# Kernel optimization log

Hardware: AMD Instinct MI355X
Metric: run time of the kernel (lower is better)

## Reference

```python
import jax, jax.numpy as jnp
import numpy as np

NC = 80
NA = 3
NO = NC + 5  # 85
ANCHORS = jnp.array([[[10.,13.],[16.,30.],[33.,23.]],
                     [[30.,61.],[62.,45.],[59.,119.]],
                     [[116.,90.],[156.,198.],[373.,326.]]], dtype=jnp.float32)
STRIDES = (8.0, 16.0, 32.0)
CONF_THRES = 0.25
IOU_THRES = 0.45
NMS_TOPK = 1000   # fixed candidate count for jit-friendly NMS (YOLO caps at max_nms)
MAX_DET = 300
MAX_WH = 4096.0   # class-offset trick from non_max_suppression


def _decode(x, w, b, anchors, stride):
    # x: [B,C,ny,nx]; w: [255,C]; 1x1 conv == channel matmul
    B, _, ny, nx = x.shape
    y = jnp.einsum('bchw,oc->bohw', x, w) + b[None, :, None, None]
    y = y.reshape(B, NA, NO, ny, nx).transpose(0, 1, 3, 4, 2)  # [B,na,ny,nx,no]
    s = jax.nn.sigmoid(y)
    yv, xv = jnp.meshgrid(jnp.arange(ny, dtype=y.dtype), jnp.arange(nx, dtype=y.dtype), indexing='ij')
    grid = jnp.stack((xv, yv), -1) - 0.5                      # [ny,nx,2]
    xy = (s[..., :2] * 2.0 + grid[None, None]) * stride
    wh = (s[..., 2:4] * 2.0) ** 2 * (anchors * stride)[None, :, None, None, :]
    out = jnp.concatenate((xy, wh, s[..., 4:]), axis=-1)
    return out.reshape(B, NA * ny * nx, NO)


def _xywh2xyxy(x):
    xy, wh = x[..., :2], x[..., 2:4]
    return jnp.concatenate([xy - wh * 0.5, xy + wh * 0.5], axis=-1)


def _box_iou(a, b):
    lt = jnp.maximum(a[:, None, :2], b[None, :, :2])
    rb = jnp.minimum(a[:, None, 2:], b[None, :, 2:])
    wh = jnp.clip(rb - lt, 0.0)
    inter = wh[..., 0] * wh[..., 1]
    area_a = (a[:, 2] - a[:, 0]) * (a[:, 3] - a[:, 1])
    area_b = (b[:, 2] - b[:, 0]) * (b[:, 3] - b[:, 1])
    return inter / (area_a[:, None] + area_b[None, :] - inter + 1e-7)


def _nms_single(pred):
    # pred: [N, 85] -> dets [MAX_DET, 6] = (x1,y1,x2,y2,conf,cls), zero-padded
    boxes = _xywh2xyxy(pred[:, :4])
    obj = pred[:, 4]
    cls_conf = pred[:, 5:] * obj[:, None]          # class scores
    score = jnp.max(cls_conf, axis=-1)
    cls = jnp.argmax(cls_conf, axis=-1)
    score = jnp.where(score > CONF_THRES, score, 0.0)
    top_s, idx = jax.lax.top_k(score, NMS_TOPK)    # fixed candidate set
    b = boxes[idx]                                  # [K,4]
    c = cls[idx].astype(b.dtype)
    bo = b + (c * MAX_WH)[:, None]                  # class-aware offset
    iou = _box_iou(bo, bo)                          # [K,K]
    keep0 = top_s > CONF_THRES
    rng = jnp.arange(NMS_TOPK)

    def body(i, keep):
        sup = (iou[i] > IOU_THRES) & (rng > i)
        return jnp.where(keep[i], keep & (~sup), keep)

    keep = jax.lax.fori_loop(0, NMS_TOPK, body, keep0)
    final_s = jnp.where(keep, top_s, 0.0)
    fs, fi = jax.lax.top_k(final_s, MAX_DET)
    det = jnp.concatenate([b[fi], fs[:, None], c[fi][:, None]], axis=-1)  # [MAX_DET,6]
    det = jnp.where((fs > CONF_THRES)[:, None], det, 0.0)
    return det


def setup_inputs() -> dict:
    key = jax.random.key(0)
    ks = jax.random.split(key, 9)
    B = 16
    return {
        'x0': jax.random.normal(ks[0], (B, 128, 80, 80), jnp.float32),
        'x1': jax.random.normal(ks[1], (B, 256, 40, 40), jnp.float32),
        'x2': jax.random.normal(ks[2], (B, 512, 20, 20), jnp.float32),
        'w0': jax.random.normal(ks[3], (255, 128), jnp.float32) * 0.02,
        'b0': jax.random.normal(ks[4], (255,), jnp.float32) * 0.02,
        'w1': jax.random.normal(ks[5], (255, 256), jnp.float32) * 0.02,
        'b1': jax.random.normal(ks[6], (255,), jnp.float32) * 0.02,
        'w2': jax.random.normal(ks[7], (255, 512), jnp.float32) * 0.02,
        'b2': jax.random.normal(ks[8], (255,), jnp.float32) * 0.02,
    }


def reference(x0, x1, x2, w0, b0, w1, b1, w2, b2):
    z0 = _decode(x0, w0, b0, ANCHORS[0], STRIDES[0])
    z1 = _decode(x1, w1, b1, ANCHORS[1], STRIDES[1])
    z2 = _decode(x2, w2, b2, ANCHORS[2], STRIDES[2])
    pred = jnp.concatenate([z0, z1, z2], axis=1)   # [B, 25200, 85]
    dets = jax.vmap(_nms_single)(pred)             # [B, 300, 6]
    return dets, pred
```

## Files before the change

kernel.cpp:

```cpp
#include <hip/hip_runtime.h>
#include <cstdint>

#define BATCH   16
#define NCLS    80
#define NOUT    85
#define NANC    3
#define NCAND   25200
#define CONF    0.25f
#define IOUT    0.45f
#define TOPK    1000
#define MAXDET  300
#define MAXWH   4096.0f
#define CAPK    2048
#define NBH     520
#define XPAD    40

typedef __attribute__((ext_vector_type(8))) short short8;
typedef __attribute__((ext_vector_type(4))) float f32x4;
typedef unsigned int u32;

constexpr size_t SCORE_OFF = 0;
constexpr size_t CLS_OFF   = SCORE_OFF + (size_t)BATCH * NCAND * 4;
constexpr size_t THR_OFF   = CLS_OFF   + (size_t)BATCH * NCAND * 4;
constexpr size_t CNT_OFF   = THR_OFF   + 256;
constexpr size_t KEYS_OFF  = CNT_OFF   + 256;
constexpr size_t RS_OFF    = KEYS_OFF  + (size_t)BATCH * CAPK * 8;
constexpr size_t RBOX_OFF  = RS_OFF    + (size_t)BATCH * TOPK * 4;
constexpr size_t RBO_OFF   = RBOX_OFF  + (size_t)BATCH * TOPK * 16;
constexpr size_t RCLS_OFF  = RBO_OFF   + (size_t)BATCH * TOPK * 16;
constexpr size_t SUP_OFF   = RCLS_OFF  + (size_t)BATCH * TOPK * 4;
constexpr int NL0 = 255 * 128, NL1 = 255 * 256, NL2 = 255 * 512;
constexpr int WB0 = 0, WB1 = 3 * NL0, WB2 = 3 * NL0 + 3 * NL1;

__device__ __forceinline__ ushort bf16rn(float f) {
    uint32_t u = __float_as_uint(f);
    uint32_t r = u + 0x7FFFu + ((u >> 16) & 1u);
    return (ushort)(r >> 16);
}

__device__ __forceinline__ void split3(float v, ushort& s1, ushort& s2, ushort& s3) {
    ushort h1 = bf16rn(v);
    float f1 = __uint_as_float((uint32_t)h1 << 16);
    float r1 = v - f1;
    ushort h2 = bf16rn(r1);
    float f2 = __uint_as_float((uint32_t)h2 << 16);
    ushort h3 = bf16rn(r1 - f2);
    s1 = h1; s2 = h2; s3 = h3;
}

__device__ __forceinline__ void gl_lds16(const float* g, void* l) {
    __builtin_amdgcn_global_load_lds(
        (const __attribute__((address_space(1))) u32*)g,
        (__attribute__((address_space(3))) u32*)l, 16, 0, 0);
}

__global__ __launch_bounds__(256)
void wsplit_kernel(const float* __restrict__ w0, const float* __restrict__ w1,
                   const float* __restrict__ w2, ushort* __restrict__ wsp) {
    int i = blockIdx.x * 256 + threadIdx.x;
    if (i >= NL0 + NL1 + NL2) return;
    const float* src; int idx, base, NL;
    if (i < NL0)            { src = w0; idx = i;             base = WB0; NL = NL0; }
    else if (i < NL0 + NL1) { src = w1; idx = i - NL0;       base = WB1; NL = NL1; }
    else                    { src = w2; idx = i - NL0 - NL1; base = WB2; NL = NL2; }
    ushort s1, s2, s3;
    split3(src[idx], s1, s2, s3);
    wsp[base + idx]          = s1;
    wsp[base + NL + idx]     = s2;
    wsp[base + 2 * NL + idx] = s3;
}

template<int C, int NN>
__device__ __forceinline__ void decode_level(
    const float* __restrict__ xb,
    const ushort* __restrict__ w1p, const ushort* __restrict__ w2p,
    const ushort* __restrict__ w3p, const float* __restrict__ bias,
    float* __restrict__ predB, float* __restrict__ scoreB, int* __restrict__ clsB,
    int tile, int lvlOff, float stride,
    float aw0, float ah0, float aw1, float ah1, float aw2, float ah2,
    char* xsb0, char* xsb1, ushort* x1, ushort* x2, ushort* x3, float* staged)
{
    constexpr int NPOS = NN * NN;
    constexpr int NCHUNK = C / 32;
    constexpr int MAXOFF = C * NPOS - 4;
    const int tid  = threadIdx.x;
    const int lane = tid & 63;
    const int wid  = tid >> 6;
    const int l16  = lane >> 4;
    const int lr   = lane & 15;
    const int pos0 = tile * 32;

    f32x4 acc[4][2];
#pragma unroll
    for (int nf = 0; nf < 4; nf++)
#pragma unroll
        for (int pf = 0; pf < 2; pf++) acc[nf][pf] = (f32x4){0.f, 0.f, 0.f, 0.f};

    char* xsb[2] = {xsb0, xsb1};

    {
        int kc = tid >> 3;
        int p4 = (tid & 7) * 4;
        int off = kc * NPOS + pos0 + p4;
        off = off < MAXOFF ? off : MAXOFF;
        gl_lds16(xb + off, xsb[0] + tid * 16);
    }

    for (int c = 0; c < NCHUNK; c++) {
        float* xs = (float*)xsb[c & 1];
        __syncthreads();
        if (c + 1 < NCHUNK) {
            const int k0n = (c + 1) * 32;
            int kc = tid >> 3;
            int p4 = (tid & 7) * 4;
            int off = (k0n + kc) * NPOS + pos0 + p4;
            off = off < MAXOFF ? off : MAXOFF;
            gl_lds16(xb + off, xsb[(c + 1) & 1] + tid * 16);
        }
        if (tid < 128) {
            const int sp = tid & 31;
            const int wv = tid >> 5;
            short8 s1v, s2v, s3v;
#pragma unroll
            for (int j = 0; j < 8; j++) {
                float f = xs[(wv * 8 + j) * 32 + sp];
                ushort u1, u2, u3;
                split3(f, u1, u2, u3);
                s1v[j] = (short)u1; s2v[j] = (short)u2; s3v[j] = (short)u3;
            }
            int dst = sp * XPAD + ((wv ^ ((sp >> 2) & 3)) << 3);
            *(short8*)(x1 + dst) = s1v;
            *(short8*)(x2 + dst) = s2v;
            *(short8*)(x3 + dst) = s3v;
        }
        asm volatile("s_waitcnt lgkmcnt(0)" ::: "memory");
        __builtin_amdgcn_s_barrier();
        __builtin_amdgcn_sched_barrier(0);
        short8 b1[2], b2[2], b3[2];
#pragma unroll
        for (int pf = 0; pf < 2; pf++) {
            int pr = pf * 16 + lr;
            int off = pr * XPAD + ((l16 ^ ((pr >> 2) & 3)) << 3);
            b1[pf] = *(const short8*)(x1 + off);
            b2[pf] = *(const short8*)(x2 + off);
            b3[pf] = *(const short8*)(x3 + off);
        }
        const int k0 = c * 32;
#pragma unroll
        for (int nf = 0; nf < 4; nf++) {
            int o = wid * 64 + nf * 16 + lr;
            int oc = o < 255 ? o : 254;
            size_t aoff = (size_t)oc * C + k0 + l16 * 8;
            short8 A1 = *(const short8*)(w1p + aoff);
            short8 A2 = *(const short8*)(w2p + aoff);
            short8 A3 = *(const short8*)(w3p + aoff);
#pragma unroll
            for (int pf = 0; pf < 2; pf++) {
                acc[nf][pf] = __builtin_amdgcn_mfma_f32_16x16x32_bf16(A1, b1[pf], acc[nf][pf], 0, 0, 0);
                acc[nf][pf] = __builtin_amdgcn_mfma_f32_16x16x32_bf16(A1, b2[pf], acc[nf][pf], 0, 0, 0);
                acc[nf][pf] = __builtin_amdgcn_mfma_f32_16x16x32_bf16(A2, b1[pf], acc[nf][pf], 0, 0, 0);
                acc[nf][pf] = __builtin_amdgcn_mfma_f32_16x16x32_bf16(A2, b2[pf], acc[nf][pf], 0, 0, 0);
                acc[nf][pf] = __builtin_amdgcn_mfma_f32_16x16x32_bf16(A1, b3[pf], acc[nf][pf], 0, 0, 0);
                acc[nf][pf] = __builtin_amdgcn_mfma_f32_16x16x32_bf16(A3, b1[pf], acc[nf][pf], 0, 0, 0);
            }
        }
    }

    float bv[16];
#pragma unroll
    for (int nf = 0; nf < 4; nf++)
#pragma unroll
        for (int r = 0; r < 4; r++) {
            int o = wid * 64 + nf * 16 + l16 * 4 + r;
            bv[nf * 4 + r] = (o < 255) ? bias[o] : 0.f;
        }

    const float aw[3] = {aw0, aw1, aw2};
    const float ah[3] = {ah0, ah1, ah2};
    const int validP = (NPOS - pos0) < 32 ? (NPOS - pos0) : 32;

#pragma unroll
    for (int a = 0; a < 3; a++) {
        __syncthreads();
#pragma unroll
        for (int nf = 0; nf < 4; nf++) {
#pragma unroll
            for (int r = 0; r < 4; r++) {
                int o = wid * 64 + nf * 16 + l16 * 4 + r;
                int j = o - a * 85;
                if (o < 255 && j >= 0 && j < 85) {
#pragma unroll
                    for (int pf = 0; pf < 2; pf++) {
                        int p = pf * 16 + lr;
                        int pos = pos0 + p;
                        float y = acc[nf][pf][r] + bv[nf * 4 + r];
                        float s = 1.f / (1.f + __expf(-y));
                        float val;
                        if (j == 0) {
                            int gyi = pos / NN;
                            float gx = (float)(pos - gyi * NN);
                            val = (2.f * s + gx - 0.5f) * stride;
                        } else if (j == 1) {
                            float gy = (float)(pos / NN);
                            val = (2.f * s + gy - 0.5f) * stride;
                        } else if (j == 2) {
                            float t2 = 2.f * s; val = t2 * t2 * aw[a];
                        } else if (j == 3) {
                            float t2 = 2.f * s; val = t2 * t2 * ah[a];
                        } else {
                            val = s;
                        }
                        staged[p * 85 + j] = val;
                    }
                }
            }
        }
        __syncthreads();
        size_t base = ((size_t)lvlOff + (size_t)a * NPOS + pos0) * 85;
        if (validP == 32) {
            const float4* s4 = (const float4*)staged;
            float4* d4 = (float4*)(predB + base);
            for (int q = tid; q < (32 * 85 / 4); q += 256) d4[q] = s4[q];
        } else {
            int tot = validP * 85;
            for (int q = tid; q < tot; q += 256) predB[base + q] = staged[q];
        }
        int p = tid >> 3, c8 = tid & 7;
        if (p < validP) {
            int j0 = 5 + c8 * 10;
            float best = staged[p * 85 + j0];
            int bi = c8 * 10;
#pragma unroll
            for (int jj = 1; jj < 10; jj++) {
                float vv = staged[p * 85 + j0 + jj];
                if (vv > best) { best = vv; bi = c8 * 10 + jj; }
            }
#pragma unroll
            for (int d = 1; d < 8; d <<= 1) {
                float ov = __shfl_xor(best, d);
                int   oi = __shfl_xor(bi, d);
                if (ov > best || (ov == best && oi < bi)) { best = ov; bi = oi; }
            }
            if (c8 == 0) {
                float obj = staged[p * 85 + 4];
                float sc = obj * best;
                int cand = lvlOff + a * NPOS + pos0 + p;
                scoreB[cand] = (sc > CONF) ? sc : 0.f;
                clsB[cand] = bi;
            }
        }
    }
}

__global__ __launch_bounds__(256)
void decode_all_kernel(const float* __restrict__ x0, const float* __restrict__ x1,
                       const float* __restrict__ x2,
                       const float* __restrict__ b0, const float* __restrict__ b1,
                       const float* __restrict__ b2,
                       const ushort* __restrict__ wsp,
                       float* __restrict__ pred,
                       float* __restrict__ scoreArr, int* __restrict__ clsArr)
{
    __shared__ __align__(16) char smem[15872];
    char*   xsb0 = smem;
    char*   xsb1 = smem + 4096;
    ushort* p1   = (ushort*)(smem + 8192);
    ushort* p2   = (ushort*)(smem + 10752);
    ushort* p3   = (ushort*)(smem + 13312);
    float*  staged = (float*)smem;

    const int b = blockIdx.y;
    const int t = blockIdx.x;

    float* predB  = pred + (size_t)b * NCAND * 85;
    float* scoreB = scoreArr + (size_t)b * NCAND;
    int*   clsB   = clsArr + (size_t)b * NCAND;

    if (t < 13) {
        decode_level<512, 20>(x2 + (size_t)b * 512 * 400,
                              wsp + WB2, wsp + WB2 + NL2, wsp + WB2 + 2 * NL2, b2,
                              predB, scoreB, clsB, t, 24000, 32.f,
                              3712.f, 2880.f, 4992.f, 6336.f, 11936.f, 10432.f,
                              xsb0, xsb1, p1, p2, p3, staged);
    } else if (t < 63) {
        decode_level<256, 40>(x1 + (size_t)b * 256 * 1600,
                              wsp + WB1, wsp + WB1 + NL1, wsp + WB1 + 2 * NL1, b1,
                              predB, scoreB, clsB, t - 13, 19200, 16.f,
                              480.f, 976.f, 992.f, 720.f, 944.f, 1904.f,
                              xsb0, xsb1, p1, p2, p3, staged);
    } else {
        decode_level<128, 80>(x0 + (size_t)b * 128 * 6400,
                              wsp + WB0, wsp + WB0 + NL0, wsp + WB0 + 2 * NL0, b0,
                              predB, scoreB, clsB, t - 63, 0, 8.f,
                              80.f, 104.f, 128.f, 240.f, 264.f, 184.f,
                              xsb0, xsb1, p1, p2, p3, staged);
    }
}

__global__ __launch_bounds__(1024)
void select1_kernel(const float* __restrict__ score, const float* __restrict__ pred,
                    const int* __restrict__ clsArr, int* __restrict__ nArr,
                    float* __restrict__ rs, float* __restrict__ rbox,
                    float* __restrict__ rbo, float* __restrict__ rcls) {
    int img = blockIdx.x, tid = threadIdx.x;
    __shared__ uint64_t sk[CAPK];
    __shared__ uint32_t h[NBH];
    __shared__ uint32_t sfx[1024 + 1];
    __shared__ int bucketSh;
    __shared__ uint32_t cntS;
    for (int i = tid; i < NBH; i += 1024) h[i] = 0;
    for (int i = tid; i < CAPK; i += 1024) sk[i] = 0ull;
    if (tid == 0) cntS = 0u;
    __syncthreads();
    const float* s = score + (size_t)img * NCAND;
    for (int i = tid; i < NCAND; i += 1024) {
        float v = s[i];
        if (v > CONF) {
            int bk = (int)((__float_as_uint(v) >> 15) - 0x7D00u);
            bk = bk < 0 ? 0 : (bk >= NBH ? NBH - 1 : bk);
            atomicAdd(&h[bk], 1u);
        }
    }
    __syncthreads();
    sfx[tid] = (tid < NBH) ? h[tid] : 0u;
    if (tid == 0) sfx[1024] = 0u;
    __syncthreads();
    for (int off = 1; off < 1024; off <<= 1) {
        uint32_t v = sfx[tid] + ((tid + off < 1024) ? sfx[tid + off] : 0u);
        __syncthreads();
        sfx[tid] = v;
        __syncthreads();
    }
    uint32_t M = sfx[0];
    uint32_t target = M < TOPK ? M : TOPK;
    if (M > 0 && tid < NBH && sfx[tid] >= target && sfx[tid + 1] < target)
        bucketSh = tid;
    __syncthreads();
    uint32_t thr = (M == 0) ? 0xFFFFFFFFu : ((uint32_t)(bucketSh + 0x7D00) << 15);
    for (int i = tid; i < NCAND; i += 1024) {
        float v = s[i];
        if (v > CONF) {
            uint32_t bits = __float_as_uint(v);
            if (bits >= thr) {
                uint32_t pos = atomicAdd(&cntS, 1u);
                if (pos < CAPK)
                    sk[pos] = ((uint64_t)bits << 32) | (uint32_t)(~(uint32_t)i);
            }
        }
    }
    __syncthreads();
    uint32_t n = cntS < CAPK ? cntS : CAPK;
    for (int k = 2; k <= CAPK; k <<= 1)
        for (int j = k >> 1; j > 0; j >>= 1) {
            for (int i = tid; i < CAPK; i += 1024) {
                int l = i ^ j;
                if (l > i) {
                    uint64_t a = sk[i], b = sk[l];
                    bool descRegion = ((i & k) == 0);
                    bool sw = descRegion ? (a < b) : (a > b);
                    if (sw) { sk[i] = b; sk[l] = a; }
                }
            }
            __syncthreads();
        }
    for (int r = tid; r < TOPK; r += 1024) {
        float sc = 0.f; uint32_t idx = 0;
        if (r < (int)n) {
            uint64_t key = sk[r];
            sc = __uint_as_float((uint32_t)(key >> 32));
            idx = ~(uint32_t)key;
        }
        const float* pr = pred + ((size_t)img * NCAND + idx) * 85;
        float cx = pr[0], cy = pr[1], ww = pr[2], hh = pr[3];
        float x1 = cx - ww * 0.5f, y1 = cy - hh * 0.5f;
        float x2 = cx + ww * 0.5f, y2 = cy + hh * 0.5f;
        float c = (float)clsArr[(size_t)img * NCAND + idx];
        float off = c * MAXWH;
        size_t rb = ((size_t)img * TOPK + r) * 4;
        rbox[rb + 0] = x1; rbox[rb + 1] = y1; rbox[rb + 2] = x2; rbox[rb + 3] = y2;
        rbo[rb + 0] = x1 + off; rbo[rb + 1] = y1 + off;
        rbo[rb + 2] = x2 + off; rbo[rb + 3] = y2 + off;
        rs[(size_t)img * TOPK + r] = sc;
        rcls[(size_t)img * TOPK + r] = c;
    }
    if (tid == 0) nArr[img] = (int)(n < TOPK ? n : TOPK);
}

__global__ __launch_bounds__(256)
void sup_kernel(const float* __restrict__ rbo, uint64_t* __restrict__ sup) {
    int img = blockIdx.y;
    int wid = threadIdx.x >> 6, lane = threadIdx.x & 63;
    int i = blockIdx.x * 4 + wid;
    if (i >= TOPK) return;
    const float* bi_ = rbo + ((size_t)img * TOPK + i) * 4;
    float ax1 = bi_[0], ay1 = bi_[1], ax2 = bi_[2], ay2 = bi_[3];
    float areaA = (ax2 - ax1) * (ay2 - ay1);
    for (int w = 0; w < 16; w++) {
        int j = w * 64 + lane;
        bool cond = false;
        if (j < TOPK && j > i) {
            const float* bj = rbo + ((size_t)img * TOPK + j) * 4;
            float bx1 = bj[0], by1 = bj[1], bx2 = bj[2], by2 = bj[3];
            float ltx = fmaxf(ax1, bx1), lty = fmaxf(ay1, by1);
            float rbx = fminf(ax2, bx2), rby = fminf(ay2, by2);
            float iw = fmaxf(rbx - ltx, 0.f), ih = fmaxf(rby - lty, 0.f);
            float inter = iw * ih;
            float areaB = (bx2 - bx1) * (by2 - by1);
            float iou = inter / (areaA + areaB - inter + 1e-7f);
            cond = iou > IOUT;
        }
        unsigned long long m = __ballot(cond);
        if (lane == w) sup[(((size_t)img * TOPK) + i) * 16 + w] = m;
    }
}

__global__ __launch_bounds__(64)
void greedy_final_kernel(const int* __restrict__ nArr, const uint64_t* __restrict__ sup,
                         const float* __restrict__ rbox, const float* __restrict__ rs,
                         const float* __restrict__ rcls, float* __restrict__ dets) {
    int img = blockIdx.x, lane = threadIdx.x;
    __shared__ uint32_t keep32[32];
    __shared__ uint16_t accList[64];
    __shared__ int ordL[MAXDET];
    int nkeep = nArr[img];
    for (int w = 0; w < 16; w++) {
        int r = w * 64 + lane;
        bool k = (r < TOPK) && (r < nkeep);
        unsigned long long m = __ballot(k);
        if (lane == 0) {
            keep32[2 * w]     = (uint32_t)m;
            keep32[2 * w + 1] = (uint32_t)(m >> 32);
        }
    }
    __syncthreads();
    const uint64_t* supim = sup + (size_t)img * TOPK * 16;
    int kept = 0;
    for (int wb = 0; wb < 16 && kept < MAXDET; wb++) {
        uint64_t word = ((uint64_t)keep32[2 * wb + 1] << 32) | keep32[2 * wb];
        if (!word) continue;
        uint64_t diag = 0;
        int myIdx = wb * 64 + lane;
        if (myIdx < TOPK) diag = supim[(size_t)myIdx * 16 + wb];
        uint64_t cur = word, acc = 0;
        for (int b = 0; b < 64; b++) {
            uint64_t row = __shfl(diag, b);
            if ((cur >> b) & 1ull) { acc |= 1ull << b; cur &= ~row; }
            if (!cur) break;
        }
        int nb = __popcll(acc);
        if (kept + nb > MAXDET) {
            int t = MAXDET - kept;
            bool mine = (acc >> lane) & 1ull;
            int rank = __popcll(acc & ((1ull << lane) - 1ull));
            acc = __ballot(mine && rank < t);
            nb = t;
        }
        {
            bool mine = (acc >> lane) & 1ull;
            int rank = __popcll(acc & ((1ull << lane) - 1ull));
            if (mine) {
                ordL[kept + rank] = wb * 64 + lane;
                accList[rank] = (uint16_t)(wb * 64 + lane);
            }
        }
        kept += nb;
        if (kept >= MAXDET) break;
        __syncthreads();
        int nw = 15 - wb;
        if (nw > 0 && nb > 0) {
            int P = nb * nw;
            for (int p = lane; p < P; p += 64) {
                int bi = p / nw, wq = wb + 1 + p % nw;
                int srcIdx = accList[bi];
                uint64_t row = supim[(size_t)srcIdx * 16 + wq];
                uint32_t lo = (uint32_t)row, hi = (uint32_t)(row >> 32);
                if (lo) atomicAnd(&keep32[2 * wq], ~lo);
                if (hi) atomicAnd(&keep32[2 * wq + 1], ~hi);
            }
        }
        __syncthreads();
    }
    __syncthreads();
    float* d = dets + (size_t)img * MAXDET * 6;
    for (int q = lane; q < MAXDET * 6; q += 64) d[q] = 0.f;
    __syncthreads();
    for (int r = lane; r < kept; r += 64) {
        int i = ordL[r];
        const float* bx = rbox + ((size_t)img * TOPK + i) * 4;
        d[r * 6 + 0] = bx[0]; d[r * 6 + 1] = bx[1];
        d[r * 6 + 2] = bx[2]; d[r * 6 + 3] = bx[3];
        d[r * 6 + 4] = rs[(size_t)img * TOPK + i];
        d[r * 6 + 5] = rcls[(size_t)img * TOPK + i];
    }
}

extern "C" void kernel_launch(void* const* d_in, const int* in_sizes, int n_in,
                              void* d_out, int out_size, void* d_ws, size_t ws_size,
                              hipStream_t stream) {
    const float* x0 = (const float*)d_in[0];
    const float* x1 = (const float*)d_in[1];
    const float* x2 = (const float*)d_in[2];
    const float* w0 = (const float*)d_in[3];
    const float* b0 = (const float*)d_in[4];
    const float* w1 = (const float*)d_in[5];
    const float* b1 = (const float*)d_in[6];
    const float* w2 = (const float*)d_in[7];
    const float* b2 = (const float*)d_in[8];

    float* dets = (float*)d_out;
    float* pred = dets + (size_t)BATCH * MAXDET * 6;

    char* ws = (char*)d_ws;
    float*    scoreArr = (float*)   (ws + SCORE_OFF);
    int*      clsArr   = (int*)     (ws + CLS_OFF);
    int*      nArr     = (int*)     (ws + THR_OFF);
    float*    rs       = (float*)   (ws + RS_OFF);
    float*    rbox     = (float*)   (ws + RBOX_OFF);
    float*    rbo      = (float*)   (ws + RBO_OFF);
    float*    rcls     = (float*)   (ws + RCLS_OFF);
    uint64_t* sup      = (uint64_t*)(ws + SUP_OFF);
    ushort*   wsp      = (ushort*)  (ws + SUP_OFF);

    wsplit_kernel<<<(NL0 + NL1 + NL2 + 255) / 256, 256, 0, stream>>>(w0, w1, w2, wsp);

    decode_all_kernel<<<dim3(263, BATCH), 256, 0, stream>>>(
        x0, x1, x2, b0, b1, b2, wsp, pred, scoreArr, clsArr);

    select1_kernel<<<BATCH, 1024, 0, stream>>>(scoreArr, pred, clsArr, nArr,
                                               rs, rbox, rbo, rcls);
    sup_kernel<<<dim3(250, BATCH), 256, 0, stream>>>(rbo, sup);
    greedy_final_kernel<<<BATCH, 64, 0, stream>>>(nArr, sup, rbox, rs, rcls, dets);
}
```

Baseline: 309.5 us.

## Load activations directly into registers and double the decode tile to 64 positions

```diff
diff --git a/kernel.cpp b/kernel.cpp
--- a/kernel.cpp
+++ b/kernel.cpp
@@ -13,7 +13,6 @@
 #define MAXWH   4096.0f
 #define CAPK    2048
 #define NBH     520
-#define XPAD    40
 
 typedef __attribute__((ext_vector_type(8))) short short8;
 typedef __attribute__((ext_vector_type(4))) float f32x4;
@@ -46,12 +45,6 @@
     float f2 = __uint_as_float((uint32_t)h2 << 16);
     ushort h3 = bf16rn(r1 - f2);
     s1 = h1; s2 = h2; s3 = h3;
-}
-
-__device__ __forceinline__ void gl_lds16(const float* g, void* l) {
-    __builtin_amdgcn_global_load_lds(
-        (const __attribute__((address_space(1))) u32*)g,
-        (__attribute__((address_space(3))) u32*)l, 16, 0, 0);
 }
 
 __global__ __launch_bounds__(256)
@@ -78,84 +71,63 @@
     float* __restrict__ predB, float* __restrict__ scoreB, int* __restrict__ clsB,
     int tile, int lvlOff, float stride,
     float aw0, float ah0, float aw1, float ah1, float aw2, float ah2,
-    char* xsb0, char* xsb1, ushort* x1, ushort* x2, ushort* x3, float* staged)
+    float* staged)
 {
     constexpr int NPOS = NN * NN;
     constexpr int NCHUNK = C / 32;
-    constexpr int MAXOFF = C * NPOS - 4;
     const int tid  = threadIdx.x;
     const int lane = tid & 63;
     const int wid  = tid >> 6;
     const int l16  = lane >> 4;
     const int lr   = lane & 15;
-    const int pos0 = tile * 32;
-
-    f32x4 acc[4][2];
+    const int pos0 = tile * 64;
+
+    f32x4 acc[4][4];
 #pragma unroll
     for (int nf = 0; nf < 4; nf++)
 #pragma unroll
-        for (int pf = 0; pf < 2; pf++) acc[nf][pf] = (f32x4){0.f, 0.f, 0.f, 0.f};
-
-    char* xsb[2] = {xsb0, xsb1};
-
-    {
-        int kc = tid >> 3;
-        int p4 = (tid & 7) * 4;
-        int off = kc * NPOS + pos0 + p4;
-        off = off < MAXOFF ? off : MAXOFF;
-        gl_lds16(xb + off, xsb[0] + tid * 16);
-    }
-
+        for (int pf = 0; pf < 4; pf++) acc[nf][pf] = (f32x4){0.f, 0.f, 0.f, 0.f};
+
+    const float* xcol[4];
+    bool pv[4];
+#pragma unroll
+    for (int pf = 0; pf < 4; pf++) {
+        int p = pf * 16 + lr;
+        pv[pf] = (pos0 + p) < NPOS;
+        xcol[pf] = xb + (pos0 + (pv[pf] ? p : 0));
+    }
+    const ushort* wA1[4]; const ushort* wA2[4]; const ushort* wA3[4];
+#pragma unroll
+    for (int nf = 0; nf < 4; nf++) {
+        int o = wid * 64 + nf * 16 + lr;
+        int oc = o < 255 ? o : 254;
+        wA1[nf] = w1p + (size_t)oc * C + l16 * 8;
+        wA2[nf] = w2p + (size_t)oc * C + l16 * 8;
+        wA3[nf] = w3p + (size_t)oc * C + l16 * 8;
+    }
+
+#pragma unroll 2
     for (int c = 0; c < NCHUNK; c++) {
-        float* xs = (float*)xsb[c & 1];
-        __syncthreads();
-        if (c + 1 < NCHUNK) {
-            const int k0n = (c + 1) * 32;
-            int kc = tid >> 3;
-            int p4 = (tid & 7) * 4;
-            int off = (k0n + kc) * NPOS + pos0 + p4;
-            off = off < MAXOFF ? off : MAXOFF;
-            gl_lds16(xb + off, xsb[(c + 1) & 1] + tid * 16);
-        }
-        if (tid < 128) {
-            const int sp = tid & 31;
-            const int wv = tid >> 5;
-            short8 s1v, s2v, s3v;
+        const int kbase = c * 32 + l16 * 8;
+        short8 b1[4], b2[4], b3[4];
+#pragma unroll
+        for (int pf = 0; pf < 4; pf++) {
 #pragma unroll
             for (int j = 0; j < 8; j++) {
-                float f = xs[(wv * 8 + j) * 32 + sp];
+                float xv = xcol[pf][(size_t)(kbase + j) * NPOS];
+                xv = pv[pf] ? xv : 0.f;
                 ushort u1, u2, u3;
-                split3(f, u1, u2, u3);
-                s1v[j] = (short)u1; s2v[j] = (short)u2; s3v[j] = (short)u3;
-            }
-            int dst = sp * XPAD + ((wv ^ ((sp >> 2) & 3)) << 3);
-            *(short8*)(x1 + dst) = s1v;
-            *(short8*)(x2 + dst) = s2v;
-            *(short8*)(x3 + dst) = s3v;
-        }
-        asm volatile("s_waitcnt lgkmcnt(0)" ::: "memory");
-        __builtin_amdgcn_s_barrier();
-        __builtin_amdgcn_sched_barrier(0);
-        short8 b1[2], b2[2], b3[2];
-#pragma unroll
-        for (int pf = 0; pf < 2; pf++) {
-            int pr = pf * 16 + lr;
-            int off = pr * XPAD + ((l16 ^ ((pr >> 2) & 3)) << 3);
-            b1[pf] = *(const short8*)(x1 + off);
-            b2[pf] = *(const short8*)(x2 + off);
-            b3[pf] = *(const short8*)(x3 + off);
-        }
-        const int k0 = c * 32;
+                split3(xv, u1, u2, u3);
+                b1[pf][j] = (short)u1; b2[pf][j] = (short)u2; b3[pf][j] = (short)u3;
+            }
+        }
 #pragma unroll
         for (int nf = 0; nf < 4; nf++) {
-            int o = wid * 64 + nf * 16 + lr;
-            int oc = o < 255 ? o : 254;
-            size_t aoff = (size_t)oc * C + k0 + l16 * 8;
-            short8 A1 = *(const short8*)(w1p + aoff);
-            short8 A2 = *(const short8*)(w2p + aoff);
-            short8 A3 = *(const short8*)(w3p + aoff);
-#pragma unroll
-            for (int pf = 0; pf < 2; pf++) {
+            short8 A1 = *(const short8*)(wA1[nf] + c * 32);
+            short8 A2 = *(const short8*)(wA2[nf] + c * 32);
+            short8 A3 = *(const short8*)(wA3[nf] + c * 32);
+#pragma unroll
+            for (int pf = 0; pf < 4; pf++) {
                 acc[nf][pf] = __builtin_amdgcn_mfma_f32_16x16x32_bf16(A1, b1[pf], acc[nf][pf], 0, 0, 0);
                 acc[nf][pf] = __builtin_amdgcn_mfma_f32_16x16x32_bf16(A1, b2[pf], acc[nf][pf], 0, 0, 0);
                 acc[nf][pf] = __builtin_amdgcn_mfma_f32_16x16x32_bf16(A2, b1[pf], acc[nf][pf], 0, 0, 0);
@@ -177,7 +149,7 @@
 
     const float aw[3] = {aw0, aw1, aw2};
     const float ah[3] = {ah0, ah1, ah2};
-    const int validP = (NPOS - pos0) < 32 ? (NPOS - pos0) : 32;
+    const int validP = (NPOS - pos0) < 64 ? (NPOS - pos0) : 64;
 
 #pragma unroll
     for (int a = 0; a < 3; a++) {
@@ -190,7 +162,7 @@
                 int j = o - a * 85;
                 if (o < 255 && j >= 0 && j < 85) {
 #pragma unroll
-                    for (int pf = 0; pf < 2; pf++) {
+                    for (int pf = 0; pf < 4; pf++) {
                         int p = pf * 16 + lr;
                         int pos = pos0 + p;
                         float y = acc[nf][pf][r] + bv[nf * 4 + r];
@@ -217,31 +189,31 @@
         }
         __syncthreads();
         size_t base = ((size_t)lvlOff + (size_t)a * NPOS + pos0) * 85;
-        if (validP == 32) {
+        if (validP == 64) {
             const float4* s4 = (const float4*)staged;
             float4* d4 = (float4*)(predB + base);
-            for (int q = tid; q < (32 * 85 / 4); q += 256) d4[q] = s4[q];
+            for (int q = tid; q < (64 * 85 / 4); q += 256) d4[q] = s4[q];
         } else {
             int tot = validP * 85;
             for (int q = tid; q < tot; q += 256) predB[base + q] = staged[q];
         }
-        int p = tid >> 3, c8 = tid & 7;
+        int p = tid >> 2, c4 = tid & 3;
         if (p < validP) {
-            int j0 = 5 + c8 * 10;
+            int j0 = 5 + c4 * 20;
             float best = staged[p * 85 + j0];
-            int bi = c8 * 10;
-#pragma unroll
-            for (int jj = 1; jj < 10; jj++) {
+            int bi = c4 * 20;
+#pragma unroll
+            for (int jj = 1; jj < 20; jj++) {
                 float vv = staged[p * 85 + j0 + jj];
-                if (vv > best) { best = vv; bi = c8 * 10 + jj; }
-            }
-#pragma unroll
-            for (int d = 1; d < 8; d <<= 1) {
+                if (vv > best) { best = vv; bi = c4 * 20 + jj; }
+            }
+#pragma unroll
+            for (int d = 1; d < 4; d <<= 1) {
                 float ov = __shfl_xor(best, d);
                 int   oi = __shfl_xor(bi, d);
                 if (ov > best || (ov == best && oi < bi)) { best = ov; bi = oi; }
             }
-            if (c8 == 0) {
+            if (c4 == 0) {
                 float obj = staged[p * 85 + 4];
                 float sc = obj * best;
                 int cand = lvlOff + a * NPOS + pos0 + p;
@@ -261,13 +233,7 @@
                        float* __restrict__ pred,
                        float* __restrict__ scoreArr, int* __restrict__ clsArr)
 {
-    __shared__ __align__(16) char smem[15872];
-    char*   xsb0 = smem;
-    char*   xsb1 = smem + 4096;
-    ushort* p1   = (ushort*)(smem + 8192);
-    ushort* p2   = (ushort*)(smem + 10752);
-    ushort* p3   = (ushort*)(smem + 13312);
-    float*  staged = (float*)smem;
+    __shared__ __align__(16) float staged[64 * 85];
 
     const int b = blockIdx.y;
     const int t = blockIdx.x;
@@ -276,24 +242,24 @@
     float* scoreB = scoreArr + (size_t)b * NCAND;
     int*   clsB   = clsArr + (size_t)b * NCAND;
 
-    if (t < 13) {
+    if (t < 7) {
         decode_level<512, 20>(x2 + (size_t)b * 512 * 400,
                               wsp + WB2, wsp + WB2 + NL2, wsp + WB2 + 2 * NL2, b2,
                               predB, scoreB, clsB, t, 24000, 32.f,
                               3712.f, 2880.f, 4992.f, 6336.f, 11936.f, 10432.f,
-                              xsb0, xsb1, p1, p2, p3, staged);
-    } else if (t < 63) {
+                              staged);
+    } else if (t < 32) {
         decode_level<256, 40>(x1 + (size_t)b * 256 * 1600,
                               wsp + WB1, wsp + WB1 + NL1, wsp + WB1 + 2 * NL1, b1,
-                              predB, scoreB, clsB, t - 13, 19200, 16.f,
+                              predB, scoreB, clsB, t - 7, 19200, 16.f,
                               480.f, 976.f, 992.f, 720.f, 944.f, 1904.f,
-                              xsb0, xsb1, p1, p2, p3, staged);
+                              staged);
     } else {
         decode_level<128, 80>(x0 + (size_t)b * 128 * 6400,
                               wsp + WB0, wsp + WB0 + NL0, wsp + WB0 + 2 * NL0, b0,
-                              predB, scoreB, clsB, t - 63, 0, 8.f,
+                              predB, scoreB, clsB, t - 32, 0, 8.f,
                               80.f, 104.f, 128.f, 240.f, 264.f, 184.f,
-                              xsb0, xsb1, p1, p2, p3, staged);
+                              staged);
     }
 }
 
@@ -523,7 +489,7 @@
 
     wsplit_kernel<<<(NL0 + NL1 + NL2 + 255) / 256, 256, 0, stream>>>(w0, w1, w2, wsp);
 
-    decode_all_kernel<<<dim3(263, BATCH), 256, 0, stream>>>(
+    decode_all_kernel<<<dim3(132, BATCH), 256, 0, stream>>>(
         x0, x1, x2, b0, b1, b2, wsp, pred, scoreArr, clsArr);
 
     select1_kernel<<<BATCH, 1024, 0, stream>>>(scoreArr, pred, clsArr, nArr,
```

Result: slower. 447.9 us (+44.7%).
